# Kernel optimization log

Measured on AMD Instinct MI355X. Metric: run time of the kernel, lower is better.

Reference implementation:

```python
import jax, jax.numpy as jnp
import numpy as np

N, E, F, H, R, NB, G, C = 100000, 500000, 128, 64, 16, 30, 1000, 10


def setup_inputs() -> dict:
    key = jax.random.key(0)
    ks = jax.random.split(key, 12)
    s = 0.05
    x = jax.random.normal(ks[0], (N, F), jnp.float32)
    edge_index = jax.random.randint(ks[1], (2, E), 0, N, dtype=jnp.int32)
    edge_norm = jax.random.uniform(ks[2], (E,), jnp.float32)
    edge_type = jax.random.randint(ks[3], (E,), 0, R, dtype=jnp.int32)
    seq_lengths = jnp.full((G,), N // G, dtype=jnp.int32)  # 1000 graphs x 100 nodes
    return dict(
        x=x, edge_index=edge_index, edge_norm=edge_norm, edge_type=edge_type,
        seq_lengths=seq_lengths, avec=0,
        w1_rel=jax.random.normal(ks[4], (F, H), jnp.float32) * s,
        w1_root=jax.random.normal(ks[5], (F, H), jnp.float32) * s,
        b1=jnp.zeros((H,), jnp.float32),
        bases=jax.random.normal(ks[6], (NB, H, H), jnp.float32) * s,
        comp=jax.random.normal(ks[7], (R, NB), jnp.float32) * s,
        w2_root=jax.random.normal(ks[8], (H, H), jnp.float32) * s,
        b2=jnp.zeros((H,), jnp.float32),
        lin_w=jax.random.normal(ks[9], (2 * (F + H), H), jnp.float32) * s,
        lin_b=jnp.zeros((H,), jnp.float32),
        fc_w=jax.random.normal(ks[10], (H, C), jnp.float32) * s,
        fc_b=jnp.zeros((C,), jnp.float32),
    )


def reference(x, edge_index, edge_norm, edge_type, seq_lengths, avec,
              w1_rel, w1_root, b1, bases, comp, w2_root, b2,
              lin_w, lin_b, fc_w, fc_b):
    src, dst = edge_index[0], edge_index[1]

    # --- GraphConv (PyG): out_i = W_rel @ sum_{j->i} w_ji x_j + W_root x_i + b
    msg = x[src] * edge_norm[:, None]                       # [E, F]
    agg = jax.ops.segment_sum(msg, dst, num_segments=N)     # [N, F]
    h = agg @ w1_rel + x @ w1_root + b1                     # [N, H]

    # --- RGCNConv with basis decomposition, mean aggregation per relation
    W = jnp.einsum('rb,bio->rio', comp, bases)              # [R, H, H]
    hs = h[src]                                             # [E, H]
    out = h @ w2_root + b2                                  # root transform + bias
    for r in range(R):  # small fixed relation count
        m = (edge_type == r).astype(h.dtype)                # [E]
        s_r = jax.ops.segment_sum(hs * m[:, None], dst, num_segments=N)
        c_r = jax.ops.segment_sum(m, dst, num_segments=N)
        out = out + (s_r / jnp.maximum(c_r, 1.0)[:, None]) @ W[r]

    feats = jnp.concatenate([x, out], axis=-1)              # [N, F+H]

    # --- ragged per-graph sum & max pooling (replaces the Python loop)
    bounds = jnp.cumsum(seq_lengths)
    gid = jnp.searchsorted(bounds, jnp.arange(N), side='right')  # [N] graph ids
    gsum = jax.ops.segment_sum(feats, gid, num_segments=G)       # [G, F+H]
    gmax = jax.ops.segment_max(feats, gid, num_segments=G)       # [G, F+H]

    hidden = jax.nn.relu(jnp.concatenate([gsum, gmax], -1) @ lin_w + lin_b)
    # dropout is identity at inference
    logits = hidden @ fc_w + fc_b                           # [G, C]
    if avec:
        return logits
    return jax.nn.log_softmax(logits, -1)
```

## Files before the change

kernel.cpp:

```cpp
#include <hip/hip_runtime.h>
#include <hip/hip_bf16.h>

#define NN 100000
#define NE 500000
#define FD 128
#define HD 64
#define RR 16
#define NBASE 30
#define GG 1000
#define CC 10
#define NGROUP 6250
#define NBLK ((NE + 255) / 256)


typedef __attribute__((ext_vector_type(8))) short bf16x8;
typedef __attribute__((ext_vector_type(4))) float f32x4;

__device__ inline unsigned short f2b(float x) {
  __hip_bfloat16 b = __float2bfloat16(x);
  return *reinterpret_cast<unsigned short*>(&b);
}
__device__ inline float b2f(unsigned short u) {
  return __uint_as_float(((unsigned)u) << 16);
}
__device__ inline unsigned pk2(float a, float b) {
  return (unsigned)f2b(a) | ((unsigned)f2b(b) << 16);
}

__global__ void k_prep(const float* comp, const float* bases, const float* w_root,
                       const float* w_rel, const float* w2, unsigned short* Wt,
                       unsigned short* wcat, unsigned short* w2t) {
  int bx = blockIdx.x;
  if (bx < 256) {
    int idx = bx * 256 + threadIdx.x;
    int r = idx >> 12, kj = idx & 4095;
    int k = kj >> 6, n = kj & 63;
    float acc = 0.0f;
    for (int b = 0; b < NBASE; ++b)
      acc += comp[r * NBASE + b] * bases[b * 4096 + kj];
    int sk = (k & 15) * 4 + (k >> 4);
    Wt[(r << 12) + n * 64 + sk] = f2b(acc);
  } else {
    int idx = (bx - 256) * 256 + threadIdx.x;
    if (idx < 16384) {
      int n = idx >> 7, k = idx & 127;
      float v = (n < 64) ? w_root[k * 64 + n] : w_rel[k * 64 + (n - 64)];
      wcat[n * 128 + k] = f2b(v);
    } else if (idx < 16384 + 4096) {
      int i2 = idx - 16384;
      int n = i2 >> 6, k = i2 & 63;
      int sk = (k & 15) * 4 + (k >> 4);
      w2t[n * 64 + sk] = f2b(w2[k * 64 + n]);
    }
  }
}

__global__ __launch_bounds__(256) void k_proj_mfma(const float* x, const unsigned short* wcat,
                                                   const float* b1, unsigned short* hroot_bf,
                                                   unsigned short* xw_bf) {
  int wv = threadIdx.x >> 6, l = threadIdx.x & 63, m = l & 15, q = l >> 4;
  int gid = blockIdx.x * 4 + wv;
  int g = gid >> 1, half = gid & 1;
  if (g >= NGROUP) return;
  size_t n0 = (size_t)g * 16;
  const float* xr = x + (n0 + m) * FD + q * 8;
  float4 xv[8];
#pragma unroll
  for (int s = 0; s < 4; ++s) {
    xv[2 * s] = *reinterpret_cast<const float4*>(xr + s * 32);
    xv[2 * s + 1] = *reinterpret_cast<const float4*>(xr + s * 32 + 4);
  }
  f32x4 acc[4];
#pragma unroll
  for (int nt = 0; nt < 4; ++nt) acc[nt] = (f32x4){0, 0, 0, 0};
#pragma unroll
  for (int s = 0; s < 4; ++s) {
    float4 xa = xv[2 * s], xb = xv[2 * s + 1];
    bf16x8 a;
    a[0] = (short)f2b(xa.x); a[1] = (short)f2b(xa.y);
    a[2] = (short)f2b(xa.z); a[3] = (short)f2b(xa.w);
    a[4] = (short)f2b(xb.x); a[5] = (short)f2b(xb.y);
    a[6] = (short)f2b(xb.z); a[7] = (short)f2b(xb.w);
#pragma unroll
    for (int nt = 0; nt < 4; ++nt) {
      bf16x8 b = *reinterpret_cast<const bf16x8*>(
          wcat + ((half * 4 + nt) * 16 + m) * 128 + s * 32 + q * 8);
      acc[nt] = __builtin_amdgcn_mfma_f32_16x16x32_bf16(a, b, acc[nt], 0, 0, 0);
    }
  }
  float bv[4] = {0, 0, 0, 0};
  if (half == 0) {
#pragma unroll
    for (int nt = 0; nt < 4; ++nt) bv[nt] = b1[nt * 16 + m];
  }
  unsigned short* dbuf = half ? xw_bf : hroot_bf;
#pragma unroll
  for (int i = 0; i < 4; ++i) {
    size_t row = (n0 + q * 4 + i) * 64 + m * 4;
    uint2 o;
    o.x = pk2(acc[0][i] + bv[0], acc[1][i] + bv[1]);
    o.y = pk2(acc[2][i] + bv[2], acc[3][i] + bv[3]);
    *reinterpret_cast<uint2*>(dbuf + row) = o;
  }
}

__global__ void k_hists(const int* ei, const int* etype, int* bch, int* hist2) {
  __shared__ int lh[RR];
  if (threadIdx.x < RR) lh[threadIdx.x] = 0;
  __syncthreads();
  int e = blockIdx.x * 256 + threadIdx.x;
  if (e < NE) {
    int t = etype[e];
    atomicAdd(&lh[t], 1);
    atomicAdd(&hist2[ei[NE + e] * RR + t], 1);
  }
  __syncthreads();
  if (threadIdx.x < RR) bch[blockIdx.x * RR + threadIdx.x] = lh[threadIdx.x];
}

__device__ inline int block_scan_incl(int v, int* ps, int t) {
  ps[t] = v;
  __syncthreads();
  for (int off = 1; off < 256; off <<= 1) {
    int u = (t >= off) ? ps[t - off] : 0;
    __syncthreads();
    ps[t] += u;
    __syncthreads();
  }
  return ps[t];
}

__global__ void k_scanA(const int* hist2, int* bsum) {
  __shared__ int red[256];
  int t = threadIdx.x;
  red[t] = hist2[blockIdx.x * 256 + t];
  __syncthreads();
  for (int s = 128; s; s >>= 1) {
    if (t < s) red[t] += red[t + s];
    __syncthreads();
  }
  if (t == 0) bsum[blockIdx.x] = red[0];
}

__global__ void k_scanB(int* bsum) {
  int t = threadIdx.x;
  int loc[25];
  int s = 0;
  if (t < 250) {
    for (int i = 0; i < 25; ++i) { loc[i] = bsum[t * 25 + i]; s += loc[i]; }
  }
  __shared__ int ps[256];
  int incl = block_scan_incl(s, ps, t);
  int base = incl - s;
  if (t < 250) {
    int run = base;
    for (int i = 0; i < 25; ++i) { int tmp = loc[i]; bsum[t * 25 + i] = run; run += tmp; }
  }
}

__global__ void k_scanC(const int* hist2, const int* bsum, int* rowptr2, int* ctr2) {
  int t = threadIdx.x;
  int gid = blockIdx.x * 256 + t;
  int v = hist2[gid];
  __shared__ int ps[256];
  int incl = block_scan_incl(v, ps, t);
  int ex = bsum[blockIdx.x] + incl - v;
  rowptr2[gid] = ex;
  ctr2[gid] = ex | (v << 20);
}

__global__ void k_bscan(const int* bch, const int* seq, int* bbase, int* offs, int* bounds) {
  __shared__ int part[16][17], chunkbase[16][17];
  __shared__ int colbase[16];
  __shared__ int ps[256];
  int t = threadIdx.x;
  int ty = t & 15, ck = t >> 4;
  const int CH = (NBLK + 15) / 16;
  int b0 = ck * CH, b1 = min(b0 + CH, NBLK);
  int s = 0;
  for (int b = b0; b < b1; ++b) s += bch[b * 16 + ty];
  part[ck][ty] = s;
  __syncthreads();
  if (t < 16) {
    int run = 0;
    for (int c = 0; c < 16; ++c) { chunkbase[c][t] = run; run += part[c][t]; }
    colbase[t] = run;
  }
  __syncthreads();
  if (t == 0) {
    int run = 0;
    for (int r = 0; r < RR; ++r) { int v = colbase[r]; offs[r] = run; colbase[r] = run; run += v; }
    offs[RR] = run;
  }
  __syncthreads();
  {
    int run = colbase[ty] + chunkbase[ck][ty];
    for (int b = b0; b < b1; ++b) {
      int v = bch[b * 16 + ty];
      bbase[b * 16 + ty] = run;
      run += v;
    }
  }
  int loc[4];
  int ss = 0;
  if (t < 250) {
    for (int i = 0; i < 4; ++i) { loc[i] = seq[t * 4 + i]; ss += loc[i]; }
  }
  int incl = block_scan_incl(ss, ps, t);
  int base = incl - ss;
  if (t < 250) {
    int run = base;
    for (int i = 0; i < 4; ++i) { run += loc[i]; bounds[t * 4 + i] = run; }
  }
}

__global__ void k_sort(const int* ei, const int* etype, const float* enorm,
                       const int* bbase, int* ctr2, uint4* tse, uint2* esen) {
  __shared__ int lcnt[RR];
  if (threadIdx.x < RR) lcnt[threadIdx.x] = 0;
  __syncthreads();
  int e = blockIdx.x * 256 + threadIdx.x;
  if (e >= NE) return;
  int t = etype[e];
  int rank = atomicAdd(&lcnt[t], 1);
  int p = bbase[blockIdx.x * RR + t] + rank;
  int src = ei[e];
  int key = ei[NE + e] * RR + t;
  int old = atomicAdd(&ctr2[key], 1);
  int pos = old & 0xFFFFF;
  int cnt = old >> 20;
  float inv = 1.0f / (float)max(cnt, 1);
  esen[pos] = make_uint2((unsigned)src, __float_as_uint(enorm[e]));
  tse[p] = make_uint4((unsigned)src, __float_as_uint(inv), (unsigned)pos, 0u);
}

__global__ __launch_bounds__(256) void k_gconv_seg(const int* rowptr2, const uint2* esen,
    const unsigned short* xw_bf, const unsigned short* hroot_bf, unsigned short* h_bf) {
  int wv = threadIdx.x >> 6, l = threadIdx.x & 63;
  int c4 = l & 15, eq = l >> 4;
  int dst = blockIdx.x * 4 + wv;
  int lo = rowptr2[dst * RR];
  int hi = (dst == NN - 1) ? NE : rowptr2[(dst + 1) * RR];
  float4 acc = {0.0f, 0.0f, 0.0f, 0.0f};
  for (int base0 = lo; base0 < hi; base0 += 64) {
    int n = min(64, hi - base0);
    int sv = 0;
    float nv = 0.0f;
    if (l < n) {
      uint2 se = esen[base0 + l];
      sv = (int)se.x;
      nv = __uint_as_float(se.y);
    }
    int k4max = (n + 3) >> 2;
    for (int k4 = 0; k4 < k4max; ++k4) {
      int eid = k4 * 4 + eq;
      int s = __shfl(sv, eid);
      float w = __shfl(nv, eid);
      if (eid < n) {
        uint2 v = *reinterpret_cast<const uint2*>(xw_bf + (size_t)s * 64 + c4 * 4);
        acc.x += b2f((unsigned short)(v.x & 0xffffu)) * w;
        acc.y += b2f((unsigned short)(v.x >> 16)) * w;
        acc.z += b2f((unsigned short)(v.y & 0xffffu)) * w;
        acc.w += b2f((unsigned short)(v.y >> 16)) * w;
      }
    }
  }
  acc.x += __shfl_xor(acc.x, 16); acc.y += __shfl_xor(acc.y, 16);
  acc.z += __shfl_xor(acc.z, 16); acc.w += __shfl_xor(acc.w, 16);
  acc.x += __shfl_xor(acc.x, 32); acc.y += __shfl_xor(acc.y, 32);
  acc.z += __shfl_xor(acc.z, 32); acc.w += __shfl_xor(acc.w, 32);
  if (l < 16) {
    uint2 hb = *reinterpret_cast<const uint2*>(hroot_bf + (size_t)dst * 64 + l * 4);
    acc.x += b2f((unsigned short)(hb.x & 0xffffu));
    acc.y += b2f((unsigned short)(hb.x >> 16));
    acc.z += b2f((unsigned short)(hb.y & 0xffffu));
    acc.w += b2f((unsigned short)(hb.y >> 16));
    uint2 o;
    o.x = pk2(acc.x, acc.y);
    o.y = pk2(acc.z, acc.w);
    *reinterpret_cast<uint2*>(h_bf + (size_t)dst * 64 + l * 4) = o;
  }
}

__global__ __launch_bounds__(256) void k_rgcn_y(const uint4* tse, const int* offs,
    const unsigned short* h_bf, const unsigned short* Wt, unsigned short* y_bf) {
  int r = blockIdx.x;
  int lo = offs[r], hi = offs[r + 1];
  int cnt = hi - lo;
  int wv = threadIdx.x >> 6;
  int l = threadIdx.x & 63;
  int m = l & 15, q = l >> 4;
  int ngroups = (cnt + 15) / 16;
  const unsigned short* Wr = Wt + (r << 12);
  bf16x8 bfr[2][4];
#pragma unroll
  for (int s = 0; s < 2; ++s)
#pragma unroll
    for (int nt = 0; nt < 4; ++nt)
      bfr[s][nt] = *reinterpret_cast<const bf16x8*>(Wr + (nt * 16 + m) * 64 + s * 32 + q * 8);

  for (int g = blockIdx.y * 4 + wv; g < ngroups; g += gridDim.y * 4) {
    int base = lo + g * 16;
    int ne = min(16, hi - base);
    int p = base + ((m < ne) ? m : 0);
    uint4 t4 = tse[p];
    int src = (int)t4.x;
    float inv = __uint_as_float(t4.y);
    int pos = (int)t4.z;
    f32x4 acc[4];
#pragma unroll
    for (int nt = 0; nt < 4; ++nt) acc[nt] = (f32x4){0, 0, 0, 0};
    const unsigned short* hrow = h_bf + (size_t)src * 64 + q * 8;
#pragma unroll
    for (int s = 0; s < 2; ++s) {
      bf16x8 afr = *reinterpret_cast<const bf16x8*>(hrow + s * 32);
#pragma unroll
      for (int nt = 0; nt < 4; ++nt)
        acc[nt] = __builtin_amdgcn_mfma_f32_16x16x32_bf16(afr, bfr[s][nt], acc[nt], 0, 0, 0);
    }
#pragma unroll
    for (int i = 0; i < 4; ++i) {
      int row = q * 4 + i;
      float ir = __shfl(inv, row);
      int pr = __shfl(pos, row);
      if (row < ne) {
        uint2 o;
        o.x = pk2(acc[0][i] * ir, acc[1][i] * ir);
        o.y = pk2(acc[2][i] * ir, acc[3][i] * ir);
        *reinterpret_cast<uint2*>(y_bf + (size_t)pr * 64 + m * 4) = o;
      }
    }
  }
}

__global__ __launch_bounds__(256) void k_out(const int* rowptr2, const unsigned short* y_bf,
    const unsigned short* h_bf, const unsigned short* w2t, const float* b2, float* out) {
  __shared__ float ldsC[16][68];
  int wv = threadIdx.x >> 6, l = threadIdx.x & 63;
  int c4 = l & 15, eq = l >> 4;
  size_t d0 = (size_t)blockIdx.x * 16;
  for (int dd = 0; dd < 4; ++dd) {
    int dst = (int)d0 + wv * 4 + dd;
    int lo = rowptr2[dst * RR];
    int hi = (dst == NN - 1) ? NE : rowptr2[(dst + 1) * RR];
    float4 acc = {0.0f, 0.0f, 0.0f, 0.0f};
    for (int row = lo + eq; row < hi; row += 4) {
      uint2 v = *reinterpret_cast<const uint2*>(y_bf + (size_t)row * 64 + c4 * 4);
      acc.x += b2f((unsigned short)(v.x & 0xffffu));
      acc.y += b2f((unsigned short)(v.x >> 16));
      acc.z += b2f((unsigned short)(v.y & 0xffffu));
      acc.w += b2f((unsigned short)(v.y >> 16));
    }
    acc.x += __shfl_xor(acc.x, 16); acc.y += __shfl_xor(acc.y, 16);
    acc.z += __shfl_xor(acc.z, 16); acc.w += __shfl_xor(acc.w, 16);
    acc.x += __shfl_xor(acc.x, 32); acc.y += __shfl_xor(acc.y, 32);
    acc.z += __shfl_xor(acc.z, 32); acc.w += __shfl_xor(acc.w, 32);
    if (l < 16)
      *reinterpret_cast<float4*>(&ldsC[wv * 4 + dd][l * 4]) = acc;
  }
  __syncthreads();
  int m = l & 15, q = l >> 4, nt = wv;
  float bb = b2[nt * 16 + m];
  f32x4 acc;
#pragma unroll
  for (int i = 0; i < 4; ++i) acc[i] = ldsC[q * 4 + i][m * 4 + nt] + bb;
#pragma unroll
  for (int s = 0; s < 2; ++s) {
    bf16x8 a = *reinterpret_cast<const bf16x8*>(h_bf + (d0 + m) * 64 + s * 32 + q * 8);
    bf16x8 b = *reinterpret_cast<const bf16x8*>(w2t + (nt * 16 + m) * 64 + s * 32 + q * 8);
    acc = __builtin_amdgcn_mfma_f32_16x16x32_bf16(a, b, acc, 0, 0, 0);
  }
#pragma unroll
  for (int i = 0; i < 4; ++i)
    out[(d0 + q * 4 + i) * 64 + nt * 16 + m] = acc[i];
}

__global__ __launch_bounds__(256) void k_head(const float* x, const float* outn,
    const int* bounds, const float* lin_w, const float* lin_b,
    const float* fc_w, const float* fc_b, float* dout) {
  __shared__ float4 psum[5][48], pmax[5][48];
  __shared__ float gsum[192], gmax[192];
  __shared__ float part[4][64];
  __shared__ float hid[HD], lg[CC], mred[2];
  int g = blockIdx.x, t = threadIdx.x;
  int lo = (g == 0) ? 0 : bounds[g - 1];
  int hi = bounds[g];
  int nn = hi - lo;
  if (t < 240) {
    int c4 = t % 48, ch = t / 48;
    int a = lo + (nn * ch) / 5, b = lo + (nn * (ch + 1)) / 5;
    float4 s = {0, 0, 0, 0};
    float4 mx = {-3.4e38f, -3.4e38f, -3.4e38f, -3.4e38f};
    const float* bp;
    int stride;
    if (c4 < 32) { bp = x + (size_t)a * FD + c4 * 4; stride = FD; }
    else         { bp = outn + (size_t)a * 64 + (c4 - 32) * 4; stride = 64; }
    int n = a;
    for (; n + 4 <= b; n += 4) {
      float4 v0 = *reinterpret_cast<const float4*>(bp);
      float4 v1 = *reinterpret_cast<const float4*>(bp + stride);
      float4 v2 = *reinterpret_cast<const float4*>(bp + 2 * stride);
      float4 v3 = *reinterpret_cast<const float4*>(bp + 3 * stride);
      bp += 4 * stride;
      s.x += v0.x + v1.x + v2.x + v3.x;
      s.y += v0.y + v1.y + v2.y + v3.y;
      s.z += v0.z + v1.z + v2.z + v3.z;
      s.w += v0.w + v1.w + v2.w + v3.w;
      mx.x = fmaxf(fmaxf(fmaxf(mx.x, v0.x), fmaxf(v1.x, v2.x)), v3.x);
      mx.y = fmaxf(fmaxf(fmaxf(mx.y, v0.y), fmaxf(v1.y, v2.y)), v3.y);
      mx.z = fmaxf(fmaxf(fmaxf(mx.z, v0.z), fmaxf(v1.z, v2.z)), v3.z);
      mx.w = fmaxf(fmaxf(fmaxf(mx.w, v0.w), fmaxf(v1.w, v2.w)), v3.w);
    }
    for (; n < b; ++n) {
      float4 v = *reinterpret_cast<const float4*>(bp);
      bp += stride;
      s.x += v.x; s.y += v.y; s.z += v.z; s.w += v.w;
      mx.x = fmaxf(mx.x, v.x); mx.y = fmaxf(mx.y, v.y);
      mx.z = fmaxf(mx.z, v.z); mx.w = fmaxf(mx.w, v.w);
    }
    psum[ch][c4] = s;
    pmax[ch][c4] = mx;
  }
  __syncthreads();
  if (t < 48) {
    float4 s = psum[0][t], m = pmax[0][t];
#pragma unroll
    for (int ch = 1; ch < 5; ++ch) {
      float4 ps = psum[ch][t], pm = pmax[ch][t];
      s.x += ps.x; s.y += ps.y; s.z += ps.z; s.w += ps.w;
      m.x = fmaxf(m.x, pm.x); m.y = fmaxf(m.y, pm.y);
      m.z = fmaxf(m.z, pm.z); m.w = fmaxf(m.w, pm.w);
    }
    gsum[t * 4 + 0] = s.x; gsum[t * 4 + 1] = s.y;
    gsum[t * 4 + 2] = s.z; gsum[t * 4 + 3] = s.w;
    gmax[t * 4 + 0] = m.x; gmax[t * 4 + 1] = m.y;
    gmax[t * 4 + 2] = m.z; gmax[t * 4 + 3] = m.w;
  }
  __syncthreads();
  {
    int o = t & 63, pp = t >> 6;
    float a = 0.0f;
    int k0 = pp * 96;
    for (int k = k0; k < k0 + 96; ++k) {
      float gv = (k < 192) ? gsum[k] : gmax[k - 192];
      a += gv * lin_w[k * 64 + o];
    }
    part[pp][o] = a;
  }
  __syncthreads();
  if (t < HD) {
    float a = lin_b[t] + part[0][t] + part[1][t] + part[2][t] + part[3][t];
    hid[t] = fmaxf(a, 0.0f);
  }
  __syncthreads();
  if (t < CC) {
    float a = fc_b[t];
    for (int k = 0; k < HD; ++k) a += hid[k] * fc_w[k * CC + t];
    lg[t] = a;
  }
  __syncthreads();
  if (t == 0) {
    float mm = lg[0];
#pragma unroll
    for (int i = 1; i < CC; ++i) mm = fmaxf(mm, lg[i]);
    float se = 0.0f;
#pragma unroll
    for (int i = 0; i < CC; ++i) se += __expf(lg[i] - mm);
    mred[0] = mm;
    mred[1] = __logf(se);
  }
  __syncthreads();
  if (t < CC) dout[g * CC + t] = lg[t] - mred[0] - mred[1];
}

extern "C" void kernel_launch(void* const* d_in, const int* in_sizes, int n_in,
                              void* d_out, int out_size, void* d_ws, size_t ws_size,
                              hipStream_t stream) {
  const float* x     = (const float*)d_in[0];
  const int* ei      = (const int*)d_in[1];
  const float* enorm = (const float*)d_in[2];
  const int* etype   = (const int*)d_in[3];
  const int* seq     = (const int*)d_in[4];
  const float* w1_rel  = (const float*)d_in[6];
  const float* w1_root = (const float*)d_in[7];
  const float* b1      = (const float*)d_in[8];
  const float* bases   = (const float*)d_in[9];
  const float* comp    = (const float*)d_in[10];
  const float* w2      = (const float*)d_in[11];
  const float* b2      = (const float*)d_in[12];
  const float* lin_w   = (const float*)d_in[13];
  const float* lin_b   = (const float*)d_in[14];
  const float* fc_w    = (const float*)d_in[15];
  const float* fc_b    = (const float*)d_in[16];
  float* dout = (float*)d_out;

  char* p = (char*)d_ws;
  unsigned short* hroot_bf = (unsigned short*)p; p += (size_t)NN * 64 * 2;
  unsigned short* xw_bf    = (unsigned short*)p; p += (size_t)NN * 64 * 2;
  float* out  = (float*)p;  p += (size_t)NN * 64 * 4;
  unsigned short* y_bf = (unsigned short*)p; p += (size_t)NE * 64 * 2;
  unsigned short* h_bf = (unsigned short*)p; p += (size_t)NN * 64 * 2;
  unsigned short* Wt   = (unsigned short*)p; p += (size_t)RR * 4096 * 2;
  unsigned short* wcat = (unsigned short*)p; p += (size_t)128 * 128 * 2;
  unsigned short* w2t  = (unsigned short*)p; p += (size_t)64 * 64 * 2;
  uint4* tse   = (uint4*)p; p += (size_t)NE * 16;
  uint2* esen  = (uint2*)p; p += (size_t)NE * 8;
  int* hist2   = (int*)p; p += (size_t)NN * RR * 4;
  int* rowptr2 = (int*)p; p += (size_t)NN * RR * 4;
  int* bch     = (int*)p; p += (size_t)NBLK * RR * 4;
  int* bbase   = (int*)p; p += (size_t)NBLK * RR * 4;
  int* bsum    = (int*)p; p += (size_t)NGROUP * 4;
  int* offs    = (int*)p; p += 68;
  int* bounds  = (int*)p; p += (size_t)GG * 4;
  int* ctr2    = (int*)out;

  hipMemsetAsync(hist2, 0, (size_t)NN * RR * 4, stream);

  hipLaunchKernelGGL(k_prep, dim3(256 + 80), dim3(256), 0, stream,
                     comp, bases, w1_root, w1_rel, w2, Wt, wcat, w2t);
  hipLaunchKernelGGL(k_proj_mfma, dim3((2 * NGROUP + 3) / 4), dim3(256), 0, stream,
                     x, wcat, b1, hroot_bf, xw_bf);
  hipLaunchKernelGGL(k_hists, dim3(NBLK), dim3(256), 0, stream, ei, etype, bch, hist2);
  hipLaunchKernelGGL(k_scanA, dim3(NGROUP), dim3(256), 0, stream, hist2, bsum);
  hipLaunchKernelGGL(k_scanB, dim3(1), dim3(256), 0, stream, bsum);
  hipLaunchKernelGGL(k_scanC, dim3(NGROUP), dim3(256), 0, stream, hist2, bsum, rowptr2, ctr2);
  hipLaunchKernelGGL(k_bscan, dim3(1), dim3(256), 0, stream, bch, seq, bbase, offs, bounds);
  hipLaunchKernelGGL(k_sort, dim3(NBLK), dim3(256), 0, stream,
                     ei, etype, enorm, bbase, ctr2, tse, esen);
  hipLaunchKernelGGL(k_gconv_seg, dim3(NN / 4), dim3(256), 0, stream,
                     rowptr2, esen, xw_bf, hroot_bf, h_bf);
  hipLaunchKernelGGL(k_rgcn_y, dim3(RR, 128), dim3(256), 0, stream,
                     tse, offs, h_bf, Wt, y_bf);
  hipLaunchKernelGGL(k_out, dim3(NN / 16), dim3(256), 0, stream,
                     rowptr2, y_bf, h_bf, w2t, b2, out);
  hipLaunchKernelGGL(k_head, dim3(GG), dim3(256), 0, stream, x, out, bounds,
                     lin_w, lin_b, fc_w, fc_b, dout);
}
```

Baseline: 360.0 us.

## Compute both projection halves per wave and prefetch next tile in persistent loop

The projection kernel now has each wave compute all 128 output columns (root and rel halves) for a 16-row group, so each x row is loaded once instead of twice. It also turns the kernel into a grid-stride persistent loop over 625 blocks that prefetches the next group's x rows while running MFMAs on the current group. The aim is to halve x reads and hide load latency. In exchange, each wave holds twice as many accumulators plus a prefetch buffer, which raises register pressure, and fewer waves are launched.

```diff
diff --git a/kernel.cpp b/kernel.cpp
--- a/kernel.cpp
+++ b/kernel.cpp
@@ -59,48 +59,66 @@
                                                    const float* b1, unsigned short* hroot_bf,
                                                    unsigned short* xw_bf) {
   int wv = threadIdx.x >> 6, l = threadIdx.x & 63, m = l & 15, q = l >> 4;
-  int gid = blockIdx.x * 4 + wv;
-  int g = gid >> 1, half = gid & 1;
+  int nw = gridDim.x * 4;
+  int g = blockIdx.x * 4 + wv;
   if (g >= NGROUP) return;
-  size_t n0 = (size_t)g * 16;
-  const float* xr = x + (n0 + m) * FD + q * 8;
+  float b1v[4];
+#pragma unroll
+  for (int nt = 0; nt < 4; ++nt) b1v[nt] = b1[nt * 16 + m];
   float4 xv[8];
-#pragma unroll
-  for (int s = 0; s < 4; ++s) {
-    xv[2 * s] = *reinterpret_cast<const float4*>(xr + s * 32);
-    xv[2 * s + 1] = *reinterpret_cast<const float4*>(xr + s * 32 + 4);
-  }
-  f32x4 acc[4];
-#pragma unroll
-  for (int nt = 0; nt < 4; ++nt) acc[nt] = (f32x4){0, 0, 0, 0};
-#pragma unroll
-  for (int s = 0; s < 4; ++s) {
-    float4 xa = xv[2 * s], xb = xv[2 * s + 1];
-    bf16x8 a;
-    a[0] = (short)f2b(xa.x); a[1] = (short)f2b(xa.y);
-    a[2] = (short)f2b(xa.z); a[3] = (short)f2b(xa.w);
-    a[4] = (short)f2b(xb.x); a[5] = (short)f2b(xb.y);
-    a[6] = (short)f2b(xb.z); a[7] = (short)f2b(xb.w);
-#pragma unroll
-    for (int nt = 0; nt < 4; ++nt) {
-      bf16x8 b = *reinterpret_cast<const bf16x8*>(
-          wcat + ((half * 4 + nt) * 16 + m) * 128 + s * 32 + q * 8);
-      acc[nt] = __builtin_amdgcn_mfma_f32_16x16x32_bf16(a, b, acc[nt], 0, 0, 0);
-    }
-  }
-  float bv[4] = {0, 0, 0, 0};
-  if (half == 0) {
-#pragma unroll
-    for (int nt = 0; nt < 4; ++nt) bv[nt] = b1[nt * 16 + m];
-  }
-  unsigned short* dbuf = half ? xw_bf : hroot_bf;
-#pragma unroll
-  for (int i = 0; i < 4; ++i) {
-    size_t row = (n0 + q * 4 + i) * 64 + m * 4;
-    uint2 o;
-    o.x = pk2(acc[0][i] + bv[0], acc[1][i] + bv[1]);
-    o.y = pk2(acc[2][i] + bv[2], acc[3][i] + bv[3]);
-    *reinterpret_cast<uint2*>(dbuf + row) = o;
+  {
+    const float* xr = x + ((size_t)g * 16 + m) * FD + q * 8;
+#pragma unroll
+    for (int s = 0; s < 4; ++s) {
+      xv[2 * s] = *reinterpret_cast<const float4*>(xr + s * 32);
+      xv[2 * s + 1] = *reinterpret_cast<const float4*>(xr + s * 32 + 4);
+    }
+  }
+  while (true) {
+    int gn = g + nw;
+    bool hn = gn < NGROUP;
+    float4 xn[8];
+    if (hn) {
+      const float* xr = x + ((size_t)gn * 16 + m) * FD + q * 8;
+#pragma unroll
+      for (int s = 0; s < 4; ++s) {
+        xn[2 * s] = *reinterpret_cast<const float4*>(xr + s * 32);
+        xn[2 * s + 1] = *reinterpret_cast<const float4*>(xr + s * 32 + 4);
+      }
+    }
+    f32x4 acc[8];
+#pragma unroll
+    for (int nt = 0; nt < 8; ++nt) acc[nt] = (f32x4){0, 0, 0, 0};
+#pragma unroll
+    for (int s = 0; s < 4; ++s) {
+      float4 xa = xv[2 * s], xb = xv[2 * s + 1];
+      bf16x8 a;
+      a[0] = (short)f2b(xa.x); a[1] = (short)f2b(xa.y);
+      a[2] = (short)f2b(xa.z); a[3] = (short)f2b(xa.w);
+      a[4] = (short)f2b(xb.x); a[5] = (short)f2b(xb.y);
+      a[6] = (short)f2b(xb.z); a[7] = (short)f2b(xb.w);
+#pragma unroll
+      for (int nt = 0; nt < 8; ++nt) {
+        bf16x8 b = *reinterpret_cast<const bf16x8*>(wcat + (nt * 16 + m) * 128 + s * 32 + q * 8);
+        acc[nt] = __builtin_amdgcn_mfma_f32_16x16x32_bf16(a, b, acc[nt], 0, 0, 0);
+      }
+    }
+    size_t n0 = (size_t)g * 16;
+#pragma unroll
+    for (int i = 0; i < 4; ++i) {
+      size_t row = (n0 + q * 4 + i) * 64 + m * 4;
+      uint2 hv, xs;
+      hv.x = pk2(acc[0][i] + b1v[0], acc[1][i] + b1v[1]);
+      hv.y = pk2(acc[2][i] + b1v[2], acc[3][i] + b1v[3]);
+      xs.x = pk2(acc[4][i], acc[5][i]);
+      xs.y = pk2(acc[6][i], acc[7][i]);
+      *reinterpret_cast<uint2*>(hroot_bf + row) = hv;
+      *reinterpret_cast<uint2*>(xw_bf + row) = xs;
+    }
+    if (!hn) break;
+#pragma unroll
+    for (int i = 0; i < 8; ++i) xv[i] = xn[i];
+    g = gn;
   }
 }
 
@@ -518,7 +536,7 @@
 
   hipLaunchKernelGGL(k_prep, dim3(256 + 80), dim3(256), 0, stream,
                      comp, bases, w1_root, w1_rel, w2, Wt, wcat, w2t);
-  hipLaunchKernelGGL(k_proj_mfma, dim3((2 * NGROUP + 3) / 4), dim3(256), 0, stream,
+  hipLaunchKernelGGL(k_proj_mfma, dim3(625), dim3(256), 0, stream,
                      x, wcat, b1, hroot_bf, xw_bf);
   hipLaunchKernelGGL(k_hists, dim3(NBLK), dim3(256), 0, stream, ei, etype, bch, hist2);
   hipLaunchKernelGGL(k_scanA, dim3(NGROUP), dim3(256), 0, stream, hist2, bsum);
```

Result: no change. 366.4 us (+1.8%).
